# Optimization experiments

Hardware: AMD Instinct MI355X
Metric: run time of the kernel (lower is better)

## Reference

```python
import jax, jax.numpy as jnp
import numpy as np

N_NODES = 100000
N_EDGES = 1600000
NFEAT = 256
NHID = 128


def setup_inputs() -> dict:
    key = jax.random.key(0)
    k1, k2, k3, k4, k5 = jax.random.split(key, 5)
    x = jax.random.normal(k1, (N_NODES, NFEAT), dtype=jnp.float32)
    edge_src = jax.random.randint(k2, (N_EDGES,), 0, N_NODES, dtype=jnp.int64)
    edge_dst = jax.random.randint(k3, (N_EDGES,), 0, N_NODES, dtype=jnp.int64)
    edge_w = jax.random.uniform(k4, (N_EDGES,), dtype=jnp.float32)
    W = jax.random.normal(k5, (NFEAT, NHID), dtype=jnp.float32) * (1.0 / np.sqrt(NFEAT))
    b = jnp.zeros((NHID,), dtype=jnp.float32)
    return {"x": x, "edge_src": edge_src, "edge_dst": edge_dst, "edge_w": edge_w, "W": W, "b": b}


def reference(x, edge_src, edge_dst, edge_w, W, b):
    # GraphConvolution: support = x @ W ; out = spmm(adj, support) + b ; then ReLU
    support = x @ W                                  # [N, nhid]
    msgs = support[edge_src] * edge_w[:, None]       # [E, nhid] gather + scale
    agg = jax.ops.segment_sum(msgs, edge_dst, num_segments=N_NODES)  # [N, nhid]
    return jax.nn.relu(agg + b)
```

## Files before the change

kernel.cpp:

```cpp
#include <hip/hip_runtime.h>
#include <hip/hip_bf16.h>

#define NFEAT 256
#define NHID  128
#define NPB   128
#define BMAX  2048
#define DCAP  3072

typedef short s16x8 __attribute__((ext_vector_type(8)));
typedef float f32x4 __attribute__((ext_vector_type(4)));
typedef float f32x2 __attribute__((ext_vector_type(2)));

static __device__ __forceinline__ ushort bfbits(float f) {
  __hip_bfloat16 h = __float2bfloat16(f);
  return *reinterpret_cast<ushort*>(&h);
}

__global__ __launch_bounds__(256) void wcvt_kernel(
    const float* __restrict__ W, ushort* __restrict__ Wt) {
  const int id = blockIdx.x * 256 + threadIdx.x;
  const int k = id >> 7, n = id & 127;
  Wt[n * NFEAT + k] = bfbits(W[id]);
}

__global__ __launch_bounds__(256) void hist_kernel(
    const int* __restrict__ edst, int* __restrict__ histT,
    int n_edges, int B, int G, int chunk) {
  __shared__ int hist[BMAX];
  const int g = blockIdx.x;
  for (int b = threadIdx.x; b < B; b += 256) hist[b] = 0;
  __syncthreads();
  const int e0 = g * chunk;
  const int e1 = (e0 + chunk < n_edges) ? e0 + chunk : n_edges;
  for (int e = e0 + threadIdx.x; e < e1; e += 256)
    atomicAdd(&hist[(uint)edst[e] >> 7], 1);
  __syncthreads();
  for (int b = threadIdx.x; b < B; b += 256) histT[(size_t)b * G + g] = hist[b];
}

__global__ __launch_bounds__(256) void scan1_kernel(
    const int* __restrict__ in, int* __restrict__ exc,
    int* __restrict__ bsums, int n) {
  const int tid = threadIdx.x;
  const int lane = tid & 63, wid = tid >> 6;
  const int base = blockIdx.x * 1024 + tid * 4;
  int v0 = 0, v1 = 0, v2 = 0, v3 = 0;
  if (base + 3 < n) {
    int4 v = *(const int4*)(in + base);
    v0 = v.x; v1 = v.y; v2 = v.z; v3 = v.w;
  } else {
    if (base + 0 < n) v0 = in[base + 0];
    if (base + 1 < n) v1 = in[base + 1];
    if (base + 2 < n) v2 = in[base + 2];
  }
  const int tsum = v0 + v1 + v2 + v3;
  int t = tsum;
#pragma unroll
  for (int d = 1; d < 64; d <<= 1) {
    int u = __shfl_up(t, d);
    if (lane >= d) t += u;
  }
  __shared__ int wtot[4], wpre[4];
  if (lane == 63) wtot[wid] = t;
  __syncthreads();
  if (tid == 0) {
    int s = 0;
    for (int w = 0; w < 4; ++w) { wpre[w] = s; s += wtot[w]; }
    bsums[blockIdx.x] = s;
  }
  __syncthreads();
  const int off = (t - tsum) + wpre[wid];
  if (base + 0 < n) exc[base + 0] = off;
  if (base + 1 < n) exc[base + 1] = off + v0;
  if (base + 2 < n) exc[base + 2] = off + v0 + v1;
  if (base + 3 < n) exc[base + 3] = off + v0 + v1 + v2;
}

__global__ __launch_bounds__(256) void scan2_kernel(int* __restrict__ bsums, int nb) {
  const int tid = threadIdx.x;
  const int lane = tid & 63, wid = tid >> 6;
  const int v = (tid < nb) ? bsums[tid] : 0;
  int t = v;
#pragma unroll
  for (int d = 1; d < 64; d <<= 1) {
    int u = __shfl_up(t, d);
    if (lane >= d) t += u;
  }
  __shared__ int wtot[4], wpre[4];
  if (lane == 63) wtot[wid] = t;
  __syncthreads();
  if (tid == 0) {
    int s = 0;
    for (int w = 0; w < 4; ++w) { wpre[w] = s; s += wtot[w]; }
  }
  __syncthreads();
  const int exc = (t - v) + wpre[wid];
  if (tid < nb) bsums[tid] = exc;
}

__global__ __launch_bounds__(256) void scan3_kernel(
    int* __restrict__ exc, const int* __restrict__ bsums,
    int* __restrict__ bucket_start, int n, int G, int B, int n_edges) {
  const int i = blockIdx.x * 256 + threadIdx.x;
  if (i < n) {
    const int v = exc[i] + bsums[i >> 10];
    exc[i] = v;
    if (i % G == 0) bucket_start[i / G] = v;
  }
  if (i == 0) bucket_start[B] = n_edges;
}

__global__ __launch_bounds__(256) void gemm_scatter_fused(
    const float* __restrict__ x, const ushort* __restrict__ Wt,
    ushort* __restrict__ sup, int n_nodes,
    const int* __restrict__ esrc, const int* __restrict__ edst,
    const float* __restrict__ ew, const int* __restrict__ base,
    int2* __restrict__ packed2, int n_edges, int B, int G, int chunk,
    int n_gemm) {
  __shared__ ushort As[64 * 64];
  __shared__ ushort Bs[128 * 64];

  const int idx = blockIdx.x;
  const long long total = (long long)n_gemm + G;
  const int c_lo = (int)((long long)idx * G / total);
  const int c_hi = (int)(((long long)idx + 1) * G / total);
  int role, sub;
  if (c_hi > c_lo) { role = 0; sub = c_lo; }
  else             { role = 1; sub = idx - c_hi; }

  if (role == 0) {
    int* cursor = (int*)As;
    const int g = sub;
    for (int b = threadIdx.x; b < B; b += 256) cursor[b] = base[(size_t)b * G + g];
    __syncthreads();
    const int e0 = g * chunk;
    const int e1 = (e0 + chunk < n_edges) ? e0 + chunk : n_edges;
    for (int e = e0 + threadIdx.x; e < e1; e += 256) {
      const int dst = edst[e];
      const int src = esrc[e];
      const float w = ew[e];
      const int pos = atomicAdd(&cursor[(uint)dst >> 7], 1);
      packed2[pos] = make_int2(src | ((dst & (NPB - 1)) << 18), __float_as_int(w));
    }
    return;
  }

  const int t = threadIdx.x;
  const int wid = t >> 6;
  const int lane = t & 63;
  const int rowBase = sub * 64;
  if (rowBase >= n_nodes) return;

  f32x4 acc[4][2];
#pragma unroll
  for (int m = 0; m < 4; ++m)
#pragma unroll
    for (int n = 0; n < 2; ++n) acc[m][n] = (f32x4){0.f, 0.f, 0.f, 0.f};

  const float4* x4 = (const float4*)x;

  for (int kc = 0; kc < 4; ++kc) {
    __syncthreads();
#pragma unroll
    for (int it = 0; it < 4; ++it) {
      const int i4 = t + it * 256;
      const int r = i4 >> 4, k4 = i4 & 15;
      const int row = rowBase + r;
      float4 v = make_float4(0.f, 0.f, 0.f, 0.f);
      if (row < n_nodes) v = x4[(size_t)row * (NFEAT / 4) + kc * 16 + k4];
      ushort4 h;
      h.x = bfbits(v.x); h.y = bfbits(v.y); h.z = bfbits(v.z); h.w = bfbits(v.w);
      int byte = (r << 7) + (k4 << 3);
      byte ^= (r & 7) << 4;
      *(ushort4*)((char*)As + byte) = h;
    }
#pragma unroll
    for (int it = 0; it < 8; ++it) {
      const int i2 = t + it * 256;
      const int col = i2 >> 4, k4 = i2 & 15;
      const ushort4 h = *(const ushort4*)(Wt + col * NFEAT + kc * 64 + k4 * 4);
      int byte = (col << 7) + (k4 << 3);
      byte ^= (col & 7) << 4;
      *(ushort4*)((char*)Bs + byte) = h;
    }
    __syncthreads();
#pragma unroll
    for (int ks = 0; ks < 2; ++ks) {
      const int k0 = ks * 32 + (lane >> 4) * 8;
      s16x8 af[4], bfr[2];
#pragma unroll
      for (int m = 0; m < 4; ++m) {
        const int r = m * 16 + (lane & 15);
        int byte = (r << 7) + (k0 << 1);
        byte ^= (r & 7) << 4;
        af[m] = *(const s16x8*)((const char*)As + byte);
      }
#pragma unroll
      for (int n = 0; n < 2; ++n) {
        const int c = wid * 32 + n * 16 + (lane & 15);
        int byte = (c << 7) + (k0 << 1);
        byte ^= (c & 7) << 4;
        bfr[n] = *(const s16x8*)((const char*)Bs + byte);
      }
#pragma unroll
      for (int m = 0; m < 4; ++m)
#pragma unroll
        for (int n = 0; n < 2; ++n)
          acc[m][n] = __builtin_amdgcn_mfma_f32_16x16x32_bf16(af[m], bfr[n], acc[m][n], 0, 0, 0);
    }
  }

#pragma unroll
  for (int m = 0; m < 4; ++m) {
#pragma unroll
    for (int rr = 0; rr < 4; ++rr) {
      const int row = rowBase + m * 16 + (lane >> 4) * 4 + rr;
      if (row < n_nodes) {
#pragma unroll
        for (int n = 0; n < 2; ++n) {
          const int col = wid * 32 + n * 16 + (lane & 15);
          sup[(size_t)row * NHID + col] = bfbits(acc[m][n][rr]);
        }
      }
    }
  }
}

__global__ __launch_bounds__(256) void bucket_agg_kernel(
    const ushort* __restrict__ sup, const int2* __restrict__ packed2,
    const int* __restrict__ bucket_start, const float* __restrict__ bias,
    float* __restrict__ out, int n_nodes) {
  __shared__ int2 list[DCAP];
  __shared__ int cnt[NPB];
  __shared__ int st[NPB];
  __shared__ int w0tot;
  const int tid = threadIdx.x;
  const int b = blockIdx.x;
  const int s0 = bucket_start[b];
  const int s1 = bucket_start[b + 1];
  const int m = s1 - s0;
  const int mm = (m < DCAP) ? m : DCAP;

  if (tid < NPB) cnt[tid] = 0;
  __syncthreads();

  int2 ev[12]; int rv[12];
#pragma unroll
  for (int j = 0; j < 12; ++j) {
    const int i = j * 256 + tid;
    if (i < mm) {
      const int2 e = packed2[s0 + i];
      ev[j] = e;
      rv[j] = atomicAdd(&cnt[((uint)e.x >> 18) & (NPB - 1)], 1);
    }
  }
  __syncthreads();

  {
    const int v = (tid < NPB) ? cnt[tid] : 0;
    int t = v;
#pragma unroll
    for (int d = 1; d < 64; d <<= 1) {
      int u = __shfl_up(t, d);
      if ((tid & 63) >= d) t += u;
    }
    if (tid == 63) w0tot = t;
    __syncthreads();
    if (tid < NPB) st[tid] = (t - v) + ((tid >= 64) ? w0tot : 0);
    __syncthreads();
  }

#pragma unroll
  for (int j = 0; j < 12; ++j) {
    const int i = j * 256 + tid;
    if (i < mm) {
      const int dl = ((uint)ev[j].x >> 18) & (NPB - 1);
      list[st[dl] + rv[j]] = ev[j];
    }
  }
  __syncthreads();

  const int wav = tid >> 6, lane = tid & 63;
  for (int nl = wav; nl < NPB; nl += 4) {
    const int node = b * NPB + nl;
    if (node >= n_nodes) break;
    const int ls = st[nl];
    const int le = ls + cnt[nl];
    float a0 = 0.f, a1 = 0.f, b0 = 0.f, b1 = 0.f;
    float c0 = 0.f, c1 = 0.f, d0 = 0.f, d1 = 0.f;
    int i = ls;
    for (; i + 7 < le; i += 8) {
      const int2 e0 = list[i + 0], e1 = list[i + 1], e2 = list[i + 2], e3 = list[i + 3];
      const int2 e4 = list[i + 4], e5 = list[i + 5], e6 = list[i + 6], e7 = list[i + 7];
      const uint u0 = *(const uint*)(sup + ((size_t)((uint)e0.x & 0x3FFFFu) << 7) + lane * 2);
      const uint u1 = *(const uint*)(sup + ((size_t)((uint)e1.x & 0x3FFFFu) << 7) + lane * 2);
      const uint u2 = *(const uint*)(sup + ((size_t)((uint)e2.x & 0x3FFFFu) << 7) + lane * 2);
      const uint u3 = *(const uint*)(sup + ((size_t)((uint)e3.x & 0x3FFFFu) << 7) + lane * 2);
      const uint u4 = *(const uint*)(sup + ((size_t)((uint)e4.x & 0x3FFFFu) << 7) + lane * 2);
      const uint u5 = *(const uint*)(sup + ((size_t)((uint)e5.x & 0x3FFFFu) << 7) + lane * 2);
      const uint u6 = *(const uint*)(sup + ((size_t)((uint)e6.x & 0x3FFFFu) << 7) + lane * 2);
      const uint u7 = *(const uint*)(sup + ((size_t)((uint)e7.x & 0x3FFFFu) << 7) + lane * 2);
      const float w0 = __int_as_float(e0.y), w1 = __int_as_float(e1.y);
      const float w2 = __int_as_float(e2.y), w3 = __int_as_float(e3.y);
      const float w4 = __int_as_float(e4.y), w5 = __int_as_float(e5.y);
      const float w6 = __int_as_float(e6.y), w7 = __int_as_float(e7.y);
      a0 += __uint_as_float(u0 << 16) * w0 + __uint_as_float(u4 << 16) * w4;
      a1 += __uint_as_float(u0 & 0xffff0000u) * w0 + __uint_as_float(u4 & 0xffff0000u) * w4;
      b0 += __uint_as_float(u1 << 16) * w1 + __uint_as_float(u5 << 16) * w5;
      b1 += __uint_as_float(u1 & 0xffff0000u) * w1 + __uint_as_float(u5 & 0xffff0000u) * w5;
      c0 += __uint_as_float(u2 << 16) * w2 + __uint_as_float(u6 << 16) * w6;
      c1 += __uint_as_float(u2 & 0xffff0000u) * w2 + __uint_as_float(u6 & 0xffff0000u) * w6;
      d0 += __uint_as_float(u3 << 16) * w3 + __uint_as_float(u7 << 16) * w7;
      d1 += __uint_as_float(u3 & 0xffff0000u) * w3 + __uint_as_float(u7 & 0xffff0000u) * w7;
    }
    for (; i < le; ++i) {
      const int2 e0 = list[i];
      const uint u0 = *(const uint*)(sup + ((size_t)((uint)e0.x & 0x3FFFFu) << 7) + lane * 2);
      const float w0 = __int_as_float(e0.y);
      a0 += __uint_as_float(u0 << 16) * w0;
      a1 += __uint_as_float(u0 & 0xffff0000u) * w0;
    }
    for (int i2 = DCAP; i2 < m; ++i2) {
      const int2 e0 = packed2[s0 + i2];
      if ((((uint)e0.x >> 18) & (NPB - 1)) == (uint)nl) {
        const uint u0 = *(const uint*)(sup + ((size_t)((uint)e0.x & 0x3FFFFu) << 7) + lane * 2);
        const float w0 = __int_as_float(e0.y);
        a0 += __uint_as_float(u0 << 16) * w0;
        a1 += __uint_as_float(u0 & 0xffff0000u) * w0;
      }
    }
    const float2 bb = ((const float2*)bias)[lane];
    f32x2 r;
    r.x = fmaxf((a0 + b0) + (c0 + d0) + bb.x, 0.f);
    r.y = fmaxf((a1 + b1) + (c1 + d1) + bb.y, 0.f);
    __builtin_nontemporal_store(r, (f32x2*)out + (size_t)node * (NHID / 2) + lane);
  }
}

__global__ __launch_bounds__(256) void scatter_bf16_kernel(
    const ushort* __restrict__ sup, const int* __restrict__ esrc,
    const int* __restrict__ edst, const float* __restrict__ ew,
    float* __restrict__ out, int n_edges) {
  const long long idx = (long long)blockIdx.x * 256 + threadIdx.x;
  const int e = (int)(idx >> 6);
  const int c2 = (int)(idx & 63);
  if (e >= n_edges) return;
  const int s = esrc[e];
  const int d = edst[e];
  const float wt = ew[e];
  const uint u = *(const uint*)(sup + (size_t)s * NHID + c2 * 2);
  float* drow = out + (size_t)d * NHID + c2 * 2;
  atomicAdd(drow + 0, __uint_as_float(u << 16) * wt);
  atomicAdd(drow + 1, __uint_as_float(u & 0xffff0000u) * wt);
}

__global__ __launch_bounds__(256) void bias_relu_kernel(
    float* __restrict__ out, const float* __restrict__ b, int n4) {
  const int i = blockIdx.x * 256 + threadIdx.x;
  if (i >= n4) return;
  float4 v = ((float4*)out)[i];
  const float4 bb = ((const float4*)b)[i & (NHID / 4 - 1)];
  v.x = fmaxf(v.x + bb.x, 0.f);
  v.y = fmaxf(v.y + bb.y, 0.f);
  v.z = fmaxf(v.z + bb.z, 0.f);
  v.w = fmaxf(v.w + bb.w, 0.f);
  ((float4*)out)[i] = v;
}

static inline size_t align_up(size_t v, size_t a) { return (v + a - 1) & ~(a - 1); }

extern "C" void kernel_launch(void* const* d_in, const int* in_sizes, int n_in,
                              void* d_out, int out_size, void* d_ws, size_t ws_size,
                              hipStream_t stream) {
  const float* x    = (const float*)d_in[0];
  const int*   esrc = (const int*)d_in[1];
  const int*   edst = (const int*)d_in[2];
  const float* ew   = (const float*)d_in[3];
  const float* W    = (const float*)d_in[4];
  const float* b    = (const float*)d_in[5];
  float* out = (float*)d_out;

  const int n_nodes = in_sizes[0] / NFEAT;
  const int n_edges = in_sizes[1];

  const int B = (n_nodes + NPB - 1) / NPB;
  int G = (n_edges + 8191) / 8192;
  const int Gmax = (256 * 1024) / (B > 0 ? B : 1);
  if (G > Gmax) G = Gmax;
  if (G < 1) G = 1;
  const int chunk = (int)align_up((size_t)(n_edges + G - 1) / G, 256);
  G = (n_edges + chunk - 1) / chunk;

  char* ws = (char*)d_ws;
  size_t off = 0;
  ushort* sup       = (ushort*)(ws + off); off = align_up(off + (size_t)n_nodes * NHID * 2, 256);
  ushort* Wt        = (ushort*)(ws + off); off = align_up(off + (size_t)NFEAT * NHID * 2, 256);
  int* histT        = (int*)(ws + off);    off = align_up(off + (size_t)B * G * 4, 256);
  int* exc          = (int*)(ws + off);    off = align_up(off + (size_t)B * G * 4, 256);
  int* bsums        = (int*)(ws + off);    off = align_up(off + 1024 * 4, 256);
  int* bucket_start = (int*)(ws + off);    off = align_up(off + ((size_t)B + 1) * 4, 256);
  int2* packed2     = (int2*)(ws + off);   off = align_up(off + (size_t)n_edges * 8, 256);
  const bool csr_ok = (off <= ws_size) && (n_nodes <= 256 * 1024) && (B <= BMAX);

  const int n_gemm = (n_nodes + 63) / 64;

  if (csr_ok) {
    wcvt_kernel<<<(NFEAT * NHID) / 256, 256, 0, stream>>>(W, Wt);

    hist_kernel<<<G, 256, 0, stream>>>(edst, histT, n_edges, B, G, chunk);

    const int n_scan = B * G;
    const int nb = (n_scan + 1023) / 1024;
    scan1_kernel<<<nb, 256, 0, stream>>>(histT, exc, bsums, n_scan);
    scan2_kernel<<<1, 256, 0, stream>>>(bsums, nb);
    scan3_kernel<<<(n_scan + 255) / 256, 256, 0, stream>>>(exc, bsums, bucket_start, n_scan, G, B, n_edges);

    gemm_scatter_fused<<<n_gemm + G, 256, 0, stream>>>(
        x, Wt, sup, n_nodes, esrc, edst, ew, exc, packed2,
        n_edges, B, G, chunk, n_gemm);

    bucket_agg_kernel<<<B, 256, 0, stream>>>(sup, packed2, bucket_start, b, out, n_nodes);
  } else {
    wcvt_kernel<<<(NFEAT * NHID) / 256, 256, 0, stream>>>(W, Wt);
    gemm_scatter_fused<<<n_gemm, 256, 0, stream>>>(
        x, Wt, sup, n_nodes, esrc, edst, ew, (int*)d_ws, (int2*)d_ws,
        0, 1, 0, 1, n_gemm);
    hipMemsetAsync(out, 0, (size_t)n_nodes * NHID * sizeof(float), stream);
    const long long threads = (long long)n_edges * 64;
    scatter_bf16_kernel<<<(int)((threads + 255) / 256), 256, 0, stream>>>(sup, esrc, edst, ew, out, n_edges);
    const int n4 = n_nodes * NHID / 4;
    bias_relu_kernel<<<(n4 + 255) / 256, 256, 0, stream>>>(out, b, n4);
  }
}
```

Baseline: 167.1 us.

## Split bucket aggregation into CSR build kernel and per-node wave aggregation kernel

The fused bucket kernel, which sorted each 128-node bucket in LDS and then aggregated with only 4 waves per block, is replaced by two kernels. A build kernel writes a fully node-sorted edge array and a per-node row_start table to global memory. A separate aggregation kernel then assigns one wave per node across many small blocks, to raise parallelism and occupancy and drop the DCAP overflow path. The cost is an extra global write and read of the edge array plus one more launch, and the build kernel's atomic-ordered placement is no longer deterministic within a node.

```diff
diff --git a/kernel.cpp b/kernel.cpp
--- a/kernel.cpp
+++ b/kernel.cpp
@@ -5,7 +5,6 @@
 #define NHID  128
 #define NPB   128
 #define BMAX  2048
-#define DCAP  3072
 
 typedef short s16x8 __attribute__((ext_vector_type(8)));
 typedef float f32x4 __attribute__((ext_vector_type(4)));
@@ -226,34 +225,25 @@
   }
 }
 
-__global__ __launch_bounds__(256) void bucket_agg_kernel(
-    const ushort* __restrict__ sup, const int2* __restrict__ packed2,
-    const int* __restrict__ bucket_start, const float* __restrict__ bias,
-    float* __restrict__ out, int n_nodes) {
-  __shared__ int2 list[DCAP];
+__global__ __launch_bounds__(256) void bucket_build_kernel(
+    const int2* __restrict__ packed2, const int* __restrict__ bucket_start,
+    int2* __restrict__ packedN, int* __restrict__ row_start,
+    int n_nodes, int n_edges) {
   __shared__ int cnt[NPB];
   __shared__ int st[NPB];
+  __shared__ int cur[NPB];
   __shared__ int w0tot;
   const int tid = threadIdx.x;
   const int b = blockIdx.x;
   const int s0 = bucket_start[b];
   const int s1 = bucket_start[b + 1];
   const int m = s1 - s0;
-  const int mm = (m < DCAP) ? m : DCAP;
 
   if (tid < NPB) cnt[tid] = 0;
   __syncthreads();
 
-  int2 ev[12]; int rv[12];
-#pragma unroll
-  for (int j = 0; j < 12; ++j) {
-    const int i = j * 256 + tid;
-    if (i < mm) {
-      const int2 e = packed2[s0 + i];
-      ev[j] = e;
-      rv[j] = atomicAdd(&cnt[((uint)e.x >> 18) & (NPB - 1)], 1);
-    }
-  }
+  for (int i = tid; i < m; i += 256)
+    atomicAdd(&cnt[((uint)packed2[s0 + i].x >> 18) & (NPB - 1)], 1);
   __syncthreads();
 
   {
@@ -266,75 +256,100 @@
     }
     if (tid == 63) w0tot = t;
     __syncthreads();
-    if (tid < NPB) st[tid] = (t - v) + ((tid >= 64) ? w0tot : 0);
+    if (tid < NPB) {
+      const int s = (t - v) + ((tid >= 64) ? w0tot : 0);
+      st[tid] = s;
+      cur[tid] = s;
+    }
     __syncthreads();
   }
 
-#pragma unroll
-  for (int j = 0; j < 12; ++j) {
-    const int i = j * 256 + tid;
-    if (i < mm) {
-      const int dl = ((uint)ev[j].x >> 18) & (NPB - 1);
-      list[st[dl] + rv[j]] = ev[j];
-    }
-  }
-  __syncthreads();
-
-  const int wav = tid >> 6, lane = tid & 63;
-  for (int nl = wav; nl < NPB; nl += 4) {
-    const int node = b * NPB + nl;
-    if (node >= n_nodes) break;
-    const int ls = st[nl];
-    const int le = ls + cnt[nl];
-    float a0 = 0.f, a1 = 0.f, b0 = 0.f, b1 = 0.f;
-    float c0 = 0.f, c1 = 0.f, d0 = 0.f, d1 = 0.f;
-    int i = ls;
-    for (; i + 7 < le; i += 8) {
-      const int2 e0 = list[i + 0], e1 = list[i + 1], e2 = list[i + 2], e3 = list[i + 3];
-      const int2 e4 = list[i + 4], e5 = list[i + 5], e6 = list[i + 6], e7 = list[i + 7];
-      const uint u0 = *(const uint*)(sup + ((size_t)((uint)e0.x & 0x3FFFFu) << 7) + lane * 2);
-      const uint u1 = *(const uint*)(sup + ((size_t)((uint)e1.x & 0x3FFFFu) << 7) + lane * 2);
-      const uint u2 = *(const uint*)(sup + ((size_t)((uint)e2.x & 0x3FFFFu) << 7) + lane * 2);
-      const uint u3 = *(const uint*)(sup + ((size_t)((uint)e3.x & 0x3FFFFu) << 7) + lane * 2);
-      const uint u4 = *(const uint*)(sup + ((size_t)((uint)e4.x & 0x3FFFFu) << 7) + lane * 2);
-      const uint u5 = *(const uint*)(sup + ((size_t)((uint)e5.x & 0x3FFFFu) << 7) + lane * 2);
-      const uint u6 = *(const uint*)(sup + ((size_t)((uint)e6.x & 0x3FFFFu) << 7) + lane * 2);
-      const uint u7 = *(const uint*)(sup + ((size_t)((uint)e7.x & 0x3FFFFu) << 7) + lane * 2);
-      const float w0 = __int_as_float(e0.y), w1 = __int_as_float(e1.y);
-      const float w2 = __int_as_float(e2.y), w3 = __int_as_float(e3.y);
-      const float w4 = __int_as_float(e4.y), w5 = __int_as_float(e5.y);
-      const float w6 = __int_as_float(e6.y), w7 = __int_as_float(e7.y);
-      a0 += __uint_as_float(u0 << 16) * w0 + __uint_as_float(u4 << 16) * w4;
-      a1 += __uint_as_float(u0 & 0xffff0000u) * w0 + __uint_as_float(u4 & 0xffff0000u) * w4;
-      b0 += __uint_as_float(u1 << 16) * w1 + __uint_as_float(u5 << 16) * w5;
-      b1 += __uint_as_float(u1 & 0xffff0000u) * w1 + __uint_as_float(u5 & 0xffff0000u) * w5;
-      c0 += __uint_as_float(u2 << 16) * w2 + __uint_as_float(u6 << 16) * w6;
-      c1 += __uint_as_float(u2 & 0xffff0000u) * w2 + __uint_as_float(u6 & 0xffff0000u) * w6;
-      d0 += __uint_as_float(u3 << 16) * w3 + __uint_as_float(u7 << 16) * w7;
-      d1 += __uint_as_float(u3 & 0xffff0000u) * w3 + __uint_as_float(u7 & 0xffff0000u) * w7;
-    }
-    for (; i < le; ++i) {
-      const int2 e0 = list[i];
-      const uint u0 = *(const uint*)(sup + ((size_t)((uint)e0.x & 0x3FFFFu) << 7) + lane * 2);
-      const float w0 = __int_as_float(e0.y);
-      a0 += __uint_as_float(u0 << 16) * w0;
-      a1 += __uint_as_float(u0 & 0xffff0000u) * w0;
-    }
-    for (int i2 = DCAP; i2 < m; ++i2) {
-      const int2 e0 = packed2[s0 + i2];
-      if ((((uint)e0.x >> 18) & (NPB - 1)) == (uint)nl) {
-        const uint u0 = *(const uint*)(sup + ((size_t)((uint)e0.x & 0x3FFFFu) << 7) + lane * 2);
-        const float w0 = __int_as_float(e0.y);
-        a0 += __uint_as_float(u0 << 16) * w0;
-        a1 += __uint_as_float(u0 & 0xffff0000u) * w0;
-      }
-    }
-    const float2 bb = ((const float2*)bias)[lane];
-    f32x2 r;
-    r.x = fmaxf((a0 + b0) + (c0 + d0) + bb.x, 0.f);
-    r.y = fmaxf((a1 + b1) + (c1 + d1) + bb.y, 0.f);
-    __builtin_nontemporal_store(r, (f32x2*)out + (size_t)node * (NHID / 2) + lane);
-  }
+  for (int i = tid; i < m; i += 256) {
+    const int2 e = packed2[s0 + i];
+    const int dl = ((uint)e.x >> 18) & (NPB - 1);
+    const int pos = atomicAdd(&cur[dl], 1);
+    packedN[s0 + pos] = e;
+  }
+
+  if (tid < NPB) {
+    const int node = b * NPB + tid;
+    if (node < n_nodes) row_start[node] = s0 + st[tid];
+  }
+  if (b == 0 && tid == 0) row_start[n_nodes] = n_edges;
+}
+
+__global__ __launch_bounds__(256) void agg_kernel(
+    const ushort* __restrict__ sup, const int2* __restrict__ packed,
+    const int* __restrict__ row_start, const float* __restrict__ bias,
+    float* __restrict__ out, int n_nodes) {
+  const int node = blockIdx.x * 4 + (threadIdx.x >> 6);
+  if (node >= n_nodes) return;
+  const int lane = threadIdx.x & 63;
+  const int start = __builtin_amdgcn_readfirstlane(row_start[node]);
+  const int end   = __builtin_amdgcn_readfirstlane(row_start[node + 1]);
+
+  float a0 = 0.f, a1 = 0.f, b0 = 0.f, b1 = 0.f;
+  float c0 = 0.f, c1 = 0.f, d0 = 0.f, d1 = 0.f;
+  int i = start;
+  for (; i + 7 < end; i += 8) {
+    const int2 e0 = packed[i + 0];
+    const int2 e1 = packed[i + 1];
+    const int2 e2 = packed[i + 2];
+    const int2 e3 = packed[i + 3];
+    const int2 e4 = packed[i + 4];
+    const int2 e5 = packed[i + 5];
+    const int2 e6 = packed[i + 6];
+    const int2 e7 = packed[i + 7];
+    const uint u0 = *(const uint*)(sup + ((size_t)((uint)e0.x & 0x3FFFFu) << 7) + lane * 2);
+    const uint u1 = *(const uint*)(sup + ((size_t)((uint)e1.x & 0x3FFFFu) << 7) + lane * 2);
+    const uint u2 = *(const uint*)(sup + ((size_t)((uint)e2.x & 0x3FFFFu) << 7) + lane * 2);
+    const uint u3 = *(const uint*)(sup + ((size_t)((uint)e3.x & 0x3FFFFu) << 7) + lane * 2);
+    const uint u4 = *(const uint*)(sup + ((size_t)((uint)e4.x & 0x3FFFFu) << 7) + lane * 2);
+    const uint u5 = *(const uint*)(sup + ((size_t)((uint)e5.x & 0x3FFFFu) << 7) + lane * 2);
+    const uint u6 = *(const uint*)(sup + ((size_t)((uint)e6.x & 0x3FFFFu) << 7) + lane * 2);
+    const uint u7 = *(const uint*)(sup + ((size_t)((uint)e7.x & 0x3FFFFu) << 7) + lane * 2);
+    const float w0 = __int_as_float(e0.y), w1 = __int_as_float(e1.y);
+    const float w2 = __int_as_float(e2.y), w3 = __int_as_float(e3.y);
+    const float w4 = __int_as_float(e4.y), w5 = __int_as_float(e5.y);
+    const float w6 = __int_as_float(e6.y), w7 = __int_as_float(e7.y);
+    a0 += __uint_as_float(u0 << 16) * w0 + __uint_as_float(u4 << 16) * w4;
+    a1 += __uint_as_float(u0 & 0xffff0000u) * w0 + __uint_as_float(u4 & 0xffff0000u) * w4;
+    b0 += __uint_as_float(u1 << 16) * w1 + __uint_as_float(u5 << 16) * w5;
+    b1 += __uint_as_float(u1 & 0xffff0000u) * w1 + __uint_as_float(u5 & 0xffff0000u) * w5;
+    c0 += __uint_as_float(u2 << 16) * w2 + __uint_as_float(u6 << 16) * w6;
+    c1 += __uint_as_float(u2 & 0xffff0000u) * w2 + __uint_as_float(u6 & 0xffff0000u) * w6;
+    d0 += __uint_as_float(u3 << 16) * w3 + __uint_as_float(u7 << 16) * w7;
+    d1 += __uint_as_float(u3 & 0xffff0000u) * w3 + __uint_as_float(u7 & 0xffff0000u) * w7;
+  }
+  for (; i + 3 < end; i += 4) {
+    const int2 e0 = packed[i + 0];
+    const int2 e1 = packed[i + 1];
+    const int2 e2 = packed[i + 2];
+    const int2 e3 = packed[i + 3];
+    const uint u0 = *(const uint*)(sup + ((size_t)((uint)e0.x & 0x3FFFFu) << 7) + lane * 2);
+    const uint u1 = *(const uint*)(sup + ((size_t)((uint)e1.x & 0x3FFFFu) << 7) + lane * 2);
+    const uint u2 = *(const uint*)(sup + ((size_t)((uint)e2.x & 0x3FFFFu) << 7) + lane * 2);
+    const uint u3 = *(const uint*)(sup + ((size_t)((uint)e3.x & 0x3FFFFu) << 7) + lane * 2);
+    const float w0 = __int_as_float(e0.y), w1 = __int_as_float(e1.y);
+    const float w2 = __int_as_float(e2.y), w3 = __int_as_float(e3.y);
+    a0 += __uint_as_float(u0 << 16) * w0 + __uint_as_float(u2 << 16) * w2;
+    a1 += __uint_as_float(u0 & 0xffff0000u) * w0 + __uint_as_float(u2 & 0xffff0000u) * w2;
+    b0 += __uint_as_float(u1 << 16) * w1 + __uint_as_float(u3 << 16) * w3;
+    b1 += __uint_as_float(u1 & 0xffff0000u) * w1 + __uint_as_float(u3 & 0xffff0000u) * w3;
+  }
+  for (; i < end; ++i) {
+    const int2 e0 = packed[i];
+    const uint u0 = *(const uint*)(sup + ((size_t)((uint)e0.x & 0x3FFFFu) << 7) + lane * 2);
+    const float w0 = __int_as_float(e0.y);
+    a0 += __uint_as_float(u0 << 16) * w0;
+    a1 += __uint_as_float(u0 & 0xffff0000u) * w0;
+  }
+
+  const float2 bb = ((const float2*)bias)[lane];
+  f32x2 r;
+  r.x = fmaxf((a0 + b0) + (c0 + d0) + bb.x, 0.f);
+  r.y = fmaxf((a1 + b1) + (c1 + d1) + bb.y, 0.f);
+  __builtin_nontemporal_store(r, (f32x2*)out + (size_t)node * (NHID / 2) + lane);
 }
 
 __global__ __launch_bounds__(256) void scatter_bf16_kernel(
@@ -399,7 +414,9 @@
   int* exc          = (int*)(ws + off);    off = align_up(off + (size_t)B * G * 4, 256);
   int* bsums        = (int*)(ws + off);    off = align_up(off + 1024 * 4, 256);
   int* bucket_start = (int*)(ws + off);    off = align_up(off + ((size_t)B + 1) * 4, 256);
+  int* row_start    = (int*)(ws + off);    off = align_up(off + ((size_t)n_nodes + 1) * 4, 256);
   int2* packed2     = (int2*)(ws + off);   off = align_up(off + (size_t)n_edges * 8, 256);
+  int2* packedN     = (int2*)(ws + off);   off = align_up(off + (size_t)n_edges * 8, 256);
   const bool csr_ok = (off <= ws_size) && (n_nodes <= 256 * 1024) && (B <= BMAX);
 
   const int n_gemm = (n_nodes + 63) / 64;
@@ -419,7 +436,10 @@
         x, Wt, sup, n_nodes, esrc, edst, ew, exc, packed2,
         n_edges, B, G, chunk, n_gemm);
 
-    bucket_agg_kernel<<<B, 256, 0, stream>>>(sup, packed2, bucket_start, b, out, n_nodes);
+    bucket_build_kernel<<<B, 256, 0, stream>>>(
+        packed2, bucket_start, packedN, row_start, n_nodes, n_edges);
+
+    agg_kernel<<<(n_nodes + 3) / 4, 256, 0, stream>>>(sup, packedN, row_start, b, out, n_nodes);
   } else {
     wcvt_kernel<<<(NFEAT * NHID) / 256, 256, 0, stream>>>(W, Wt);
     gemm_scatter_fused<<<n_gemm, 256, 0, stream>>>(
```

Result: faster. 146.5 us (-12.3%).
